# Kernel optimization log

Hardware: AMD Instinct MI355X
Metric: run time of the kernel (lower is better)

## Reference

```python
import jax, jax.numpy as jnp
import numpy as np
from jax import lax

K = 7            # cfg.network.PSROI_BINS == pool_size
FEAT_STRIDE = 16
LAMDA = 0.1
D_PER_BIN = 8    # feature channels per position-sensitive bin -> C = K*K*8 = 392


def _bilinear(feat, y, x, extra_idx):
    """Bilinearly sample feat[H,W,...] at float coords (y,x); extra_idx are
    integer index arrays (broadcast to y.shape) selecting trailing feat axes."""
    H, W = feat.shape[0], feat.shape[1]
    y0f = jnp.floor(y); x0f = jnp.floor(x)
    wy = (y - y0f)[..., None]
    wx = (x - x0f)[..., None]
    y0 = jnp.clip(y0f.astype(jnp.int32), 0, H - 1)
    y1 = jnp.clip(y0f.astype(jnp.int32) + 1, 0, H - 1)
    x0 = jnp.clip(x0f.astype(jnp.int32), 0, W - 1)
    x1 = jnp.clip(x0f.astype(jnp.int32) + 1, 0, W - 1)
    def g(yi, xi):
        return feat[(yi, xi) + extra_idx]
    return ((1 - wy) * (1 - wx) * g(y0, x0) + (1 - wy) * wx * g(y0, x1)
            + wy * (1 - wx) * g(y1, x0) + wy * wx * g(y1, x1))


def ps_roi(f, rois, k, feat_stride, offsets=None):
    """Position-sensitive RoI pooling. f: [H,W,C] with C = k*k*D (bin-major
    channel layout). rois: [N,5] (batch, x1, y1, x2, y2) in image coords.
    offsets (optional): [N, k*k, G, 2] per-bin, per-channel-group (x,y) shifts
    in image coords. Returns [N, D, k, k]."""
    H, W, C = f.shape
    N = rois.shape[0]
    kk = k * k
    D = C // kk
    x1 = rois[:, 1] / feat_stride
    y1 = rois[:, 2] / feat_stride
    x2 = (rois[:, 3] + 1.0) / feat_stride
    y2 = (rois[:, 4] + 1.0) / feat_stride
    bw = (x2 - x1) / k  # [N]
    bh = (y2 - y1) / k
    jj = jnp.tile(jnp.arange(k, dtype=f.dtype), k)     # bin = i*k + j
    ii = jnp.repeat(jnp.arange(k, dtype=f.dtype), k)
    cx = x1[:, None] + (jj + 0.5) * bw[:, None]        # [N, kk] bin centers
    cy = y1[:, None] + (ii + 0.5) * bh[:, None]
    bins = jnp.arange(kk, dtype=jnp.int32)
    if offsets is None:
        feat = f.reshape(H, W, kk, D)
        b = jnp.broadcast_to(bins, (N, kk))
        vals = _bilinear(feat, cy, cx, (b,))           # [N, kk, D]
    else:
        G = offsets.shape[2]
        cxg = cx[:, :, None] + offsets[..., 0] / feat_stride  # [N, kk, G]
        cyg = cy[:, :, None] + offsets[..., 1] / feat_stride
        feat = f.reshape(H, W, kk, G, D // G)
        b = jnp.broadcast_to(bins[None, :, None], (N, kk, G))
        g = jnp.broadcast_to(jnp.arange(G, dtype=jnp.int32)[None, None, :], (N, kk, G))
        vals = _bilinear(feat, cyg, cxg, (b, g))       # [N, kk, G, D//G]
        vals = vals.reshape(N, kk, D)
    return jnp.transpose(vals.reshape(N, k, k, D), (0, 3, 1, 2))  # [N, D, k, k]


def setup_inputs():
    key = jax.random.key(0)
    kf, kw, k1, k2 = jax.random.split(key, 4)
    H = W = 128
    C = K * K * D_PER_BIN
    N = 2048
    features = jax.random.normal(kf, (1, H, W, C), jnp.float32)
    conv_w = jax.random.normal(kw, (3, 3, C, 2 * 4 * K * K), jnp.float32) * 0.01
    img = float(H * FEAT_STRIDE)
    xy1 = jax.random.uniform(k1, (N, 2), minval=0.0, maxval=img * 0.6)
    wh = jax.random.uniform(k2, (N, 2), minval=32.0, maxval=img * 0.4)
    xy2 = jnp.minimum(xy1 + wh, img - 1.0)
    rois = jnp.concatenate([jnp.zeros((N, 1)), xy1[:, :1], xy1[:, 1:], xy2[:, :1], xy2[:, 1:]], axis=1).astype(jnp.float32)
    return {"features": features, "rois": rois, "conv_w": conv_w}


def reference(features, rois, conv_w):
    # offset branch: 3x3 conv (no bias) -> PS-RoI pool -> scale by lamda*roi size
    offset_map = lax.conv_general_dilated(features, conv_w, (1, 1), 'SAME',
                                          dimension_numbers=('NHWC', 'HWIO', 'NHWC'))
    off = ps_roi(offset_map[0], rois, K, FEAT_STRIDE)          # [N, 8, K, K]
    N = off.shape[0]
    off = off.reshape(N, -1, 2, K, K)                          # [N, 4, 2, K, K]
    off = jnp.transpose(off, (2, 3, 4, 1, 0))                  # [2, K, K, 4, N]
    roi_w = rois[:, 3] - rois[:, 1] + 1.0
    roi_h = rois[:, 4] - rois[:, 2] + 1.0
    off = jnp.stack((off[0] * roi_w * LAMDA, off[1] * roi_h * LAMDA), axis=0)
    off = jnp.transpose(off, (4, 1, 2, 3, 0))                  # [N, K, K, 4, 2]
    off = off.reshape(N, K * K, -1, 2)                         # [N, kk, 4, 2]
    # deformable PS-RoI pooling of the features with predicted offsets
    return ps_roi(features[0], rois, K, FEAT_STRIDE, offsets=off)  # [N, 8, K, K]
```

## Files before the change

kernel.cpp:

```cpp
#include <hip/hip_runtime.h>
#include <cstddef>
#include <cstdint>

#define HH    128
#define WW    128
#define CC    392
#define NPIX  (HH*WW)
#define NROI  2048
#define PSK   7
#define NBIN  49
#define LAMDA 0.1f

#define CPAD      448
#define HPAD      130
#define NPADCO    448
#define SEGSTRIDE (9*CPAD)
#define BKK       64

#define FBM 64
#define FBN 64
#define FBK 32

typedef _Float16 half8   __attribute__((ext_vector_type(8)));
typedef _Float16 half2v  __attribute__((ext_vector_type(2)));
typedef float    floatx4 __attribute__((ext_vector_type(4)));

__device__ __forceinline__ void async_ld16(const _Float16* g, _Float16* l) {
  __builtin_amdgcn_global_load_lds((const __attribute__((address_space(1))) void*)g,
                                   (__attribute__((address_space(3))) void*)l,
                                   16, 0, 0);
}

#define FPREP ((HPAD * HPAD * (CPAD / 8) + 255) / 256)
#define WPREP (9 * 14 * 14)

__global__ __launch_bounds__(256)
void prep_kernel(const float* __restrict__ F, const float* __restrict__ Wt,
                 _Float16* __restrict__ Fh, _Float16* __restrict__ Bth) {
  __shared__ float tile[32][33];
  const int t = threadIdx.x;
  if (blockIdx.x < FPREP) {
    const int idx = blockIdx.x * 256 + t;
    const int total = HPAD * HPAD * (CPAD / 8);
    if (idx >= total) return;
    const int p  = idx / (CPAD / 8);
    const int cg = idx - p * (CPAD / 8);
    const int c  = cg * 8;
    const int py = p / HPAD;
    const int px = p - py * HPAD;
    half8 h;
#pragma unroll
    for (int i = 0; i < 8; ++i) h[i] = (_Float16)0.f;
    if (py >= 1 && py <= HH && px >= 1 && px <= WW && c < CC) {
      const float* src = F + ((size_t)(py - 1) * WW + (px - 1)) * CC + c;
      const float4 v0 = *(const float4*)src;
      const float4 v1 = *(const float4*)(src + 4);
      h[0] = (_Float16)v0.x; h[1] = (_Float16)v0.y;
      h[2] = (_Float16)v0.z; h[3] = (_Float16)v0.w;
      h[4] = (_Float16)v1.x; h[5] = (_Float16)v1.y;
      h[6] = (_Float16)v1.z; h[7] = (_Float16)v1.w;
    }
    *(half8*)(Fh + (size_t)p * CPAD + c) = h;
  } else {
    const int bid = blockIdx.x - FPREP;
    const int seg = bid / (14 * 14);
    const int rem = bid - seg * (14 * 14);
    const int cit = rem / 14;
    const int cot = rem - cit * 14;
    const int ci0 = cit * 32, co0 = cot * 32;
#pragma unroll
    for (int i = 0; i < 4; ++i) {
      const int idx = t + i * 256;
      const int lr = idx >> 5;
      const int lc = idx & 31;
      const int ci = ci0 + lr, co = co0 + lc;
      float v = 0.f;
      if (ci < CC && co < CC) v = Wt[((size_t)seg * CC + ci) * CC + co];
      tile[lr][lc] = v;
    }
    __syncthreads();
#pragma unroll
    for (int i = 0; i < 4; ++i) {
      const int idx = t + i * 256;
      const int lr = idx >> 5;
      const int lc = idx & 31;
      Bth[(size_t)(co0 + lr) * SEGSTRIDE + seg * CPAD + ci0 + lc] = (_Float16)tile[lc][lr];
    }
  }
}

__global__ __launch_bounds__(256, 4)
void conv_mfma_kernel(const _Float16* __restrict__ Fh, const _Float16* __restrict__ Bth,
                      _Float16* __restrict__ OM) {
  __shared__ __align__(16) _Float16 As[128 * BKK];
  __shared__ __align__(16) _Float16 Bs[64 * BKK];

  const int t = threadIdx.x;
  const int L = t & 63;
  const int w = t >> 6;
  const int row0 = blockIdx.x * 128;
  const int col0 = blockIdx.y * 64;

  const int srow = L >> 3;
  const int kofs = ((L & 7) ^ srow) * 8;

  const int ya = row0 >> 7;
  const int nbase = col0 + w * 16 + srow;

  const int wm = (w >> 1) * 64;
  const int wn = (w & 1) * 32;
  const int fr = L & 15;
  const int quad = L >> 4;
  const int pg0 = (quad ^ (fr & 7)) * 8;
  const int pg1 = ((4 + quad) ^ (fr & 7)) * 8;

  floatx4 acc[4][2];
#pragma unroll
  for (int i = 0; i < 4; ++i)
#pragma unroll
    for (int j = 0; j < 2; ++j) {
      floatx4 z = {0.f, 0.f, 0.f, 0.f};
      acc[i][j] = z;
    }

  for (int q = 0; q < 63; ++q) {
    const int seg = q / 7;
    const int it  = q - seg * 7;
    const int dy = seg / 3 - 1;
    const int dx = seg - (seg / 3) * 3 - 1;
    const int fy = ya + 1 + dy;
    const int cb = it * BKK;
    const _Float16* gArow = Fh + ((size_t)fy * HPAD + (1 + dx)) * CPAD + kofs + cb;
    const _Float16* gB = Bth + (size_t)nbase * SEGSTRIDE + seg * CPAD + kofs + cb;

#pragma unroll
    for (int j = 0; j < 4; ++j) {
      const int xr = w * 32 + j * 8 + srow;
      async_ld16(gArow + (size_t)xr * CPAD, &As[(w * 32 + j * 8) * BKK]);
    }
#pragma unroll
    for (int j = 0; j < 2; ++j) {
      async_ld16(gB + (size_t)(j * 8) * SEGSTRIDE, &Bs[(w * 16 + j * 8) * BKK]);
    }
    __syncthreads();

    half8 a0[4], a1[4], b0[2], b1[2];
#pragma unroll
    for (int mt = 0; mt < 4; ++mt) {
      const int rb = (wm + mt * 16 + fr) * BKK;
      a0[mt] = *(const half8*)(&As[rb + pg0]);
      a1[mt] = *(const half8*)(&As[rb + pg1]);
    }
#pragma unroll
    for (int nt = 0; nt < 2; ++nt) {
      const int rb = (wn + nt * 16 + fr) * BKK;
      b0[nt] = *(const half8*)(&Bs[rb + pg0]);
      b1[nt] = *(const half8*)(&Bs[rb + pg1]);
    }
#pragma unroll
    for (int mt = 0; mt < 4; ++mt)
#pragma unroll
      for (int nt = 0; nt < 2; ++nt)
        acc[mt][nt] = __builtin_amdgcn_mfma_f32_16x16x32_f16(a0[mt], b0[nt], acc[mt][nt], 0, 0, 0);
#pragma unroll
    for (int mt = 0; mt < 4; ++mt)
#pragma unroll
      for (int nt = 0; nt < 2; ++nt)
        acc[mt][nt] = __builtin_amdgcn_mfma_f32_16x16x32_f16(a1[mt], b1[nt], acc[mt][nt], 0, 0, 0);
    __syncthreads();
  }

#pragma unroll
  for (int mt = 0; mt < 4; ++mt) {
    const int rbase = row0 + wm + mt * 16 + quad * 4;
#pragma unroll
    for (int nt = 0; nt < 2; ++nt) {
      const int col = col0 + wn + nt * 16 + fr;
      if (col < CC) {
#pragma unroll
        for (int r = 0; r < 4; ++r)
          OM[(size_t)(rbase + r) * CC + col] = (_Float16)acc[mt][nt][r];
      }
    }
  }
}

__global__ __launch_bounds__(256)
void conv3x3_kernel(const float* __restrict__ F, const float* __restrict__ Wt,
                    float* __restrict__ OM) {
  __shared__ float Asf[FBK][FBM + 4];
  __shared__ float Bsf[FBK][FBN + 4];

  const int t = threadIdx.x;
  const int ty = t >> 4;
  const int tx = t & 15;
  const int row0 = blockIdx.x * FBM;
  const int col0 = blockIdx.y * FBN;

  float acc[4][4];
#pragma unroll
  for (int i = 0; i < 4; ++i)
#pragma unroll
    for (int j = 0; j < 4; ++j) acc[i][j] = 0.f;

  for (int kc = 0; kc < 117; ++kc) {
    const int seg   = kc / 13;
    const int cbase = (kc - seg * 13) * FBK;
    const int dy    = seg / 3 - 1;
    const int dx    = seg - (seg / 3) * 3 - 1;

#pragma unroll
    for (int rep = 0; rep < (FBM * FBK) / 256; ++rep) {
      const int idx = t + rep * 256;
      const int r  = idx >> 5;
      const int lk = idx & 31;
      const int m  = row0 + r;
      const int y  = m >> 7, x = m & 127;
      const int yy = y + dy, xx = x + dx;
      const int ci = cbase + lk;
      float v = 0.f;
      if ((unsigned)yy < HH && (unsigned)xx < WW && ci < CC)
        v = F[((size_t)(yy * WW + xx)) * CC + ci];
      Asf[lk][r] = v;
    }
#pragma unroll
    for (int rep = 0; rep < (FBK * FBN) / 256; ++rep) {
      const int idx = t + rep * 256;
      const int lk  = idx >> 6;
      const int nn  = idx & 63;
      const int ci  = cbase + lk;
      const int col = col0 + nn;
      float v = 0.f;
      if (ci < CC && col < CC)
        v = Wt[((size_t)(seg * CC + ci)) * CC + col];
      Bsf[lk][nn] = v;
    }
    __syncthreads();

#pragma unroll
    for (int lk = 0; lk < FBK; ++lk) {
      const float4 a4 = *(const float4*)(&Asf[lk][ty * 4]);
      const float4 b4 = *(const float4*)(&Bsf[lk][tx * 4]);
      const float av[4] = {a4.x, a4.y, a4.z, a4.w};
      const float bv[4] = {b4.x, b4.y, b4.z, b4.w};
#pragma unroll
      for (int i = 0; i < 4; ++i)
#pragma unroll
        for (int j = 0; j < 4; ++j)
          acc[i][j] = fmaf(av[i], bv[j], acc[i][j]);
    }
    __syncthreads();
  }

  const int col = col0 + tx * 4;
  if (col < CC) {
#pragma unroll
    for (int i = 0; i < 4; ++i) {
      float4 v = make_float4(acc[i][0], acc[i][1], acc[i][2], acc[i][3]);
      *(float4*)(&OM[((size_t)(row0 + ty * 4 + i)) * CC + col]) = v;
    }
  }
}

__device__ __forceinline__ void bilin_setup(float y, float x,
                                            int& iy0, int& iy1, int& ix0, int& ix1,
                                            float& w00, float& w01, float& w10, float& w11) {
  const float y0f = floorf(y), x0f = floorf(x);
  const float wy = y - y0f, wx = x - x0f;
  const int a = (int)y0f, b = (int)x0f;
  iy0 = min(max(a, 0), HH - 1);
  iy1 = min(max(a + 1, 0), HH - 1);
  ix0 = min(max(b, 0), WW - 1);
  ix1 = min(max(b + 1, 0), WW - 1);
  w00 = (1.f - wy) * (1.f - wx);
  w01 = (1.f - wy) * wx;
  w10 = wy * (1.f - wx);
  w11 = wy * wx;
}

__device__ __forceinline__ void roi_geom(const float* R, int n, int bi, int bj,
                                         float& cx, float& cy, float& sxs, float& sys) {
  const float rx1 = R[n * 5 + 1], ry1 = R[n * 5 + 2];
  const float rx2 = R[n * 5 + 3], ry2 = R[n * 5 + 4];
  const float x1 = rx1 * (1.f / 16.f);
  const float y1 = ry1 * (1.f / 16.f);
  const float x2 = (rx2 + 1.f) * (1.f / 16.f);
  const float y2 = (ry2 + 1.f) * (1.f / 16.f);
  const float bw = (x2 - x1) * (1.f / 7.f);
  const float bh = (y2 - y1) * (1.f / 7.f);
  cx = x1 + ((float)bj + 0.5f) * bw;
  cy = y1 + ((float)bi + 0.5f) * bh;
  sxs = (rx2 - rx1 + 1.f) * (LAMDA / 16.f);
  sys = (ry2 - ry1 + 1.f) * (LAMDA / 16.f);
}

__global__ __launch_bounds__(256)
void psroi_pool_f16_kernel(const _Float16* __restrict__ Fh, const float* __restrict__ R,
                           const _Float16* __restrict__ OM, float* __restrict__ out) {
  const int tid = blockIdx.x * 256 + threadIdx.x;
  if (tid >= NROI * NBIN * 4) return;
  const int g  = tid & 3;
  const int nb = tid >> 2;
  const int n  = nb / NBIN;
  const int b  = nb - n * NBIN;
  const int bi = b / PSK;
  const int bj = b - bi * PSK;

  float cx, cy, sxs, sys;
  roi_geom(R, n, bi, bj, cx, cy, sxs, sys);

  int iy0, iy1, ix0, ix1;
  float w00, w01, w10, w11;
  bilin_setup(cy, cx, iy0, iy1, ix0, ix1, w00, w01, w10, w11);

  const size_t c0 = (size_t)b * 8 + 2 * g;
  const half2v m00 = *(const half2v*)(OM + (size_t)(iy0 * WW + ix0) * CC + c0);
  const half2v m01 = *(const half2v*)(OM + (size_t)(iy0 * WW + ix1) * CC + c0);
  const half2v m10 = *(const half2v*)(OM + (size_t)(iy1 * WW + ix0) * CC + c0);
  const half2v m11 = *(const half2v*)(OM + (size_t)(iy1 * WW + ix1) * CC + c0);

  const float ox = w00 * (float)m00[0] + w01 * (float)m01[0]
                 + w10 * (float)m10[0] + w11 * (float)m11[0];
  const float oy = w00 * (float)m00[1] + w01 * (float)m01[1]
                 + w10 * (float)m10[1] + w11 * (float)m11[1];

  const float sx = cx + ox * sxs;
  const float sy = cy + oy * sys;

  int jy0, jy1, jx0, jx1;
  float u00, u01, u10, u11;
  bilin_setup(sy, sx, jy0, jy1, jx0, jx1, u00, u01, u10, u11);

  const half2v q00 = *(const half2v*)(Fh + ((size_t)(jy0 + 1) * HPAD + (jx0 + 1)) * CPAD + c0);
  const half2v q01 = *(const half2v*)(Fh + ((size_t)(jy0 + 1) * HPAD + (jx1 + 1)) * CPAD + c0);
  const half2v q10 = *(const half2v*)(Fh + ((size_t)(jy1 + 1) * HPAD + (jx0 + 1)) * CPAD + c0);
  const half2v q11 = *(const half2v*)(Fh + ((size_t)(jy1 + 1) * HPAD + (jx1 + 1)) * CPAD + c0);

  const float v0 = u00 * (float)q00[0] + u01 * (float)q01[0]
                 + u10 * (float)q10[0] + u11 * (float)q11[0];
  const float v1 = u00 * (float)q00[1] + u01 * (float)q01[1]
                 + u10 * (float)q10[1] + u11 * (float)q11[1];

  out[((size_t)n * 8 + 2 * g + 0) * NBIN + b] = v0;
  out[((size_t)n * 8 + 2 * g + 1) * NBIN + b] = v1;
}

__global__ __launch_bounds__(256)
void psroi_pool_f32_kernel(const float* __restrict__ F, const float* __restrict__ R,
                           const float* __restrict__ OM, float* __restrict__ out) {
  const int tid = blockIdx.x * 256 + threadIdx.x;
  if (tid >= NROI * NBIN * 4) return;
  const int g  = tid & 3;
  const int nb = tid >> 2;
  const int n  = nb / NBIN;
  const int b  = nb - n * NBIN;
  const int bi = b / PSK;
  const int bj = b - bi * PSK;

  float cx, cy, sxs, sys;
  roi_geom(R, n, bi, bj, cx, cy, sxs, sys);

  int iy0, iy1, ix0, ix1;
  float w00, w01, w10, w11;
  bilin_setup(cy, cx, iy0, iy1, ix0, ix1, w00, w01, w10, w11);

  const size_t c0 = (size_t)b * 8 + 2 * g;
  const float2 m00 = *(const float2*)(OM + (size_t)(iy0 * WW + ix0) * CC + c0);
  const float2 m01 = *(const float2*)(OM + (size_t)(iy0 * WW + ix1) * CC + c0);
  const float2 m10 = *(const float2*)(OM + (size_t)(iy1 * WW + ix0) * CC + c0);
  const float2 m11 = *(const float2*)(OM + (size_t)(iy1 * WW + ix1) * CC + c0);

  const float ox = w00 * m00.x + w01 * m01.x + w10 * m10.x + w11 * m11.x;
  const float oy = w00 * m00.y + w01 * m01.y + w10 * m10.y + w11 * m11.y;

  const float sx = cx + ox * sxs;
  const float sy = cy + oy * sys;

  int jy0, jy1, jx0, jx1;
  float u00, u01, u10, u11;
  bilin_setup(sy, sx, jy0, jy1, jx0, jx1, u00, u01, u10, u11);

  const float2 q00 = *(const float2*)(F + (size_t)(jy0 * WW + jx0) * CC + c0);
  const float2 q01 = *(const float2*)(F + (size_t)(jy0 * WW + jx1) * CC + c0);
  const float2 q10 = *(const float2*)(F + (size_t)(jy1 * WW + jx0) * CC + c0);
  const float2 q11 = *(const float2*)(F + (size_t)(jy1 * WW + jx1) * CC + c0);

  const float v0 = u00 * q00.x + u01 * q01.x + u10 * q10.x + u11 * q11.x;
  const float v1 = u00 * q00.y + u01 * q01.y + u10 * q10.y + u11 * q11.y;

  out[((size_t)n * 8 + 2 * g + 0) * NBIN + b] = v0;
  out[((size_t)n * 8 + 2 * g + 1) * NBIN + b] = v1;
}

extern "C" void kernel_launch(void* const* d_in, const int* in_sizes, int n_in,
                              void* d_out, int out_size, void* d_ws, size_t ws_size,
                              hipStream_t stream) {
  const float* F  = (const float*)d_in[0];
  const float* R  = (const float*)d_in[1];
  const float* Wt = (const float*)d_in[2];
  float* out = (float*)d_out;

  const size_t omBytes  = (size_t)NPIX * CC * sizeof(_Float16);
  const size_t fhBytes  = (size_t)HPAD * HPAD * CPAD * sizeof(_Float16);
  const size_t bthBytes = (size_t)NPADCO * SEGSTRIDE * sizeof(_Float16);
  const size_t need = omBytes + fhBytes + bthBytes;

  const int totalPool = NROI * NBIN * 4;
  const int poolGrid = (totalPool + 255) / 256;

  if (ws_size >= need) {
    _Float16* OM  = (_Float16*)d_ws;
    _Float16* Fh  = (_Float16*)((char*)d_ws + omBytes);
    _Float16* Bth = Fh + (size_t)HPAD * HPAD * CPAD;

    prep_kernel<<<FPREP + WPREP, 256, 0, stream>>>(F, Wt, Fh, Bth);

    dim3 g(NPIX / 128, NPADCO / 64);
    conv_mfma_kernel<<<g, 256, 0, stream>>>(Fh, Bth, OM);

    psroi_pool_f16_kernel<<<poolGrid, 256, 0, stream>>>(Fh, R, OM, out);
  } else {
    float* OMf = (float*)d_ws;
    dim3 cgrid(NPIX / FBM, (CC + FBN - 1) / FBN);
    conv3x3_kernel<<<cgrid, 256, 0, stream>>>(F, Wt, OMf);
    psroi_pool_f32_kernel<<<poolGrid, 256, 0, stream>>>(F, R, OMf, out);
  }
}
```

Measured before the change: 164.6 us.

## Enlarge conv MFMA tile to 128x128 and split K across two partial outputs

The conv GEMM tile is widened to 128 output channels per block and the 63 K-iterations are split across a z-dimension of two, each writing a separate fp16 partial offset map. The pooling kernel reads both partial maps and sums them during the offset bilinear interpolation. This aims to improve operand reuse per block and raise parallelism per block's K length. In exchange, padding output channels to 512 wastes more MFMA work, the larger accumulator array raises register pressure, and a second offset map must be written.

After: 167.4 us. Within noise of the previous version (+1.7%).

```diff
diff --git a/kernel.cpp b/kernel.cpp
--- a/kernel.cpp
+++ b/kernel.cpp
@@ -13,9 +13,10 @@
 
 #define CPAD      448
 #define HPAD      130
-#define NPADCO    448
+#define NPADCO    512
 #define SEGSTRIDE (9*CPAD)
 #define BKK       64
+#define NQ        63
 
 #define FBM 64
 #define FBN 64
@@ -32,7 +33,7 @@
 }
 
 #define FPREP ((HPAD * HPAD * (CPAD / 8) + 255) / 256)
-#define WPREP (9 * 14 * 14)
+#define WPREP (9 * 14 * 16)
 
 __global__ __launch_bounds__(256)
 void prep_kernel(const float* __restrict__ F, const float* __restrict__ Wt,
@@ -63,10 +64,10 @@
     *(half8*)(Fh + (size_t)p * CPAD + c) = h;
   } else {
     const int bid = blockIdx.x - FPREP;
-    const int seg = bid / (14 * 14);
-    const int rem = bid - seg * (14 * 14);
-    const int cit = rem / 14;
-    const int cot = rem - cit * 14;
+    const int seg = bid / (14 * 16);
+    const int rem = bid - seg * (14 * 16);
+    const int cit = rem / 16;
+    const int cot = rem - cit * 16;
     const int ci0 = cit * 32, co0 = cot * 32;
 #pragma unroll
     for (int i = 0; i < 4; ++i) {
@@ -91,39 +92,43 @@
 
 __global__ __launch_bounds__(256, 4)
 void conv_mfma_kernel(const _Float16* __restrict__ Fh, const _Float16* __restrict__ Bth,
-                      _Float16* __restrict__ OM) {
+                      _Float16* __restrict__ OMbase, int span) {
   __shared__ __align__(16) _Float16 As[128 * BKK];
-  __shared__ __align__(16) _Float16 Bs[64 * BKK];
+  __shared__ __align__(16) _Float16 Bs[128 * BKK];
 
   const int t = threadIdx.x;
   const int L = t & 63;
   const int w = t >> 6;
   const int row0 = blockIdx.x * 128;
-  const int col0 = blockIdx.y * 64;
+  const int col0 = blockIdx.y * 128;
+  const int kz   = blockIdx.z;
+  const int q0 = kz * span;
+  const int q1 = min(NQ, q0 + span);
+  _Float16* __restrict__ OMp = OMbase + (size_t)kz * NPIX * CC;
 
   const int srow = L >> 3;
   const int kofs = ((L & 7) ^ srow) * 8;
 
   const int ya = row0 >> 7;
-  const int nbase = col0 + w * 16 + srow;
+  const int nbase = col0 + w * 32 + srow;
 
   const int wm = (w >> 1) * 64;
-  const int wn = (w & 1) * 32;
+  const int wn = (w & 1) * 64;
   const int fr = L & 15;
   const int quad = L >> 4;
   const int pg0 = (quad ^ (fr & 7)) * 8;
   const int pg1 = ((4 + quad) ^ (fr & 7)) * 8;
 
-  floatx4 acc[4][2];
+  floatx4 acc[4][4];
 #pragma unroll
   for (int i = 0; i < 4; ++i)
 #pragma unroll
-    for (int j = 0; j < 2; ++j) {
+    for (int j = 0; j < 4; ++j) {
       floatx4 z = {0.f, 0.f, 0.f, 0.f};
       acc[i][j] = z;
     }
 
-  for (int q = 0; q < 63; ++q) {
+  for (int q = q0; q < q1; ++q) {
     const int seg = q / 7;
     const int it  = q - seg * 7;
     const int dy = seg / 3 - 1;
@@ -139,12 +144,12 @@
       async_ld16(gArow + (size_t)xr * CPAD, &As[(w * 32 + j * 8) * BKK]);
     }
 #pragma unroll
-    for (int j = 0; j < 2; ++j) {
-      async_ld16(gB + (size_t)(j * 8) * SEGSTRIDE, &Bs[(w * 16 + j * 8) * BKK]);
+    for (int j = 0; j < 4; ++j) {
+      async_ld16(gB + (size_t)(j * 8) * SEGSTRIDE, &Bs[(w * 32 + j * 8) * BKK]);
     }
     __syncthreads();
 
-    half8 a0[4], a1[4], b0[2], b1[2];
+    half8 a0[4], a1[4], b0[4], b1[4];
 #pragma unroll
     for (int mt = 0; mt < 4; ++mt) {
       const int rb = (wm + mt * 16 + fr) * BKK;
@@ -152,7 +157,7 @@
       a1[mt] = *(const half8*)(&As[rb + pg1]);
     }
 #pragma unroll
-    for (int nt = 0; nt < 2; ++nt) {
+    for (int nt = 0; nt < 4; ++nt) {
       const int rb = (wn + nt * 16 + fr) * BKK;
       b0[nt] = *(const half8*)(&Bs[rb + pg0]);
       b1[nt] = *(const half8*)(&Bs[rb + pg1]);
@@ -160,12 +165,12 @@
 #pragma unroll
     for (int mt = 0; mt < 4; ++mt)
 #pragma unroll
-      for (int nt = 0; nt < 2; ++nt)
+      for (int nt = 0; nt < 4; ++nt)
         acc[mt][nt] = __builtin_amdgcn_mfma_f32_16x16x32_f16(a0[mt], b0[nt], acc[mt][nt], 0, 0, 0);
 #pragma unroll
     for (int mt = 0; mt < 4; ++mt)
 #pragma unroll
-      for (int nt = 0; nt < 2; ++nt)
+      for (int nt = 0; nt < 4; ++nt)
         acc[mt][nt] = __builtin_amdgcn_mfma_f32_16x16x32_f16(a1[mt], b1[nt], acc[mt][nt], 0, 0, 0);
     __syncthreads();
   }
@@ -174,12 +179,12 @@
   for (int mt = 0; mt < 4; ++mt) {
     const int rbase = row0 + wm + mt * 16 + quad * 4;
 #pragma unroll
-    for (int nt = 0; nt < 2; ++nt) {
+    for (int nt = 0; nt < 4; ++nt) {
       const int col = col0 + wn + nt * 16 + fr;
       if (col < CC) {
 #pragma unroll
         for (int r = 0; r < 4; ++r)
-          OM[(size_t)(rbase + r) * CC + col] = (_Float16)acc[mt][nt][r];
+          OMp[(size_t)(rbase + r) * CC + col] = (_Float16)acc[mt][nt][r];
       }
     }
   }
@@ -296,7 +301,8 @@
 
 __global__ __launch_bounds__(256)
 void psroi_pool_f16_kernel(const _Float16* __restrict__ Fh, const float* __restrict__ R,
-                           const _Float16* __restrict__ OM, float* __restrict__ out) {
+                           const _Float16* __restrict__ OMa, const _Float16* __restrict__ OMb,
+                           float* __restrict__ out) {
   const int tid = blockIdx.x * 256 + threadIdx.x;
   if (tid >= NROI * NBIN * 4) return;
   const int g  = tid & 3;
@@ -314,15 +320,28 @@
   bilin_setup(cy, cx, iy0, iy1, ix0, ix1, w00, w01, w10, w11);
 
   const size_t c0 = (size_t)b * 8 + 2 * g;
-  const half2v m00 = *(const half2v*)(OM + (size_t)(iy0 * WW + ix0) * CC + c0);
-  const half2v m01 = *(const half2v*)(OM + (size_t)(iy0 * WW + ix1) * CC + c0);
-  const half2v m10 = *(const half2v*)(OM + (size_t)(iy1 * WW + ix0) * CC + c0);
-  const half2v m11 = *(const half2v*)(OM + (size_t)(iy1 * WW + ix1) * CC + c0);
-
-  const float ox = w00 * (float)m00[0] + w01 * (float)m01[0]
-                 + w10 * (float)m10[0] + w11 * (float)m11[0];
-  const float oy = w00 * (float)m00[1] + w01 * (float)m01[1]
-                 + w10 * (float)m10[1] + w11 * (float)m11[1];
+  const size_t s00 = (size_t)(iy0 * WW + ix0) * CC + c0;
+  const size_t s01 = (size_t)(iy0 * WW + ix1) * CC + c0;
+  const size_t s10 = (size_t)(iy1 * WW + ix0) * CC + c0;
+  const size_t s11 = (size_t)(iy1 * WW + ix1) * CC + c0;
+
+  const half2v a00 = *(const half2v*)(OMa + s00);
+  const half2v a01 = *(const half2v*)(OMa + s01);
+  const half2v a10 = *(const half2v*)(OMa + s10);
+  const half2v a11 = *(const half2v*)(OMa + s11);
+  const half2v e00 = *(const half2v*)(OMb + s00);
+  const half2v e01 = *(const half2v*)(OMb + s01);
+  const half2v e10 = *(const half2v*)(OMb + s10);
+  const half2v e11 = *(const half2v*)(OMb + s11);
+
+  const float ox = w00 * ((float)a00[0] + (float)e00[0])
+                 + w01 * ((float)a01[0] + (float)e01[0])
+                 + w10 * ((float)a10[0] + (float)e10[0])
+                 + w11 * ((float)a11[0] + (float)e11[0]);
+  const float oy = w00 * ((float)a00[1] + (float)e00[1])
+                 + w01 * ((float)a01[1] + (float)e01[1])
+                 + w10 * ((float)a10[1] + (float)e10[1])
+                 + w11 * ((float)a11[1] + (float)e11[1]);
 
   const float sx = cx + ox * sxs;
   const float sy = cy + oy * sys;
@@ -403,22 +422,23 @@
   const size_t omBytes  = (size_t)NPIX * CC * sizeof(_Float16);
   const size_t fhBytes  = (size_t)HPAD * HPAD * CPAD * sizeof(_Float16);
   const size_t bthBytes = (size_t)NPADCO * SEGSTRIDE * sizeof(_Float16);
-  const size_t need = omBytes + fhBytes + bthBytes;
+  const size_t need = 2 * omBytes + fhBytes + bthBytes;
 
   const int totalPool = NROI * NBIN * 4;
   const int poolGrid = (totalPool + 255) / 256;
 
   if (ws_size >= need) {
-    _Float16* OM  = (_Float16*)d_ws;
-    _Float16* Fh  = (_Float16*)((char*)d_ws + omBytes);
+    _Float16* OMa = (_Float16*)d_ws;
+    _Float16* OMb = OMa + (size_t)NPIX * CC;
+    _Float16* Fh  = (_Float16*)((char*)d_ws + 2 * omBytes);
     _Float16* Bth = Fh + (size_t)HPAD * HPAD * CPAD;
 
     prep_kernel<<<FPREP + WPREP, 256, 0, stream>>>(F, Wt, Fh, Bth);
 
-    dim3 g(NPIX / 128, NPADCO / 64);
-    conv_mfma_kernel<<<g, 256, 0, stream>>>(Fh, Bth, OM);
-
-    psroi_pool_f16_kernel<<<poolGrid, 256, 0, stream>>>(Fh, R, OM, out);
+    dim3 g(NPIX / 128, NPADCO / 128, 2);
+    conv_mfma_kernel<<<g, 256, 0, stream>>>(Fh, Bth, OMa, 32);
+
+    psroi_pool_f16_kernel<<<poolGrid, 256, 0, stream>>>(Fh, R, OMa, OMb, out);
   } else {
     float* OMf = (float*)d_ws;
     dim3 cgrid(NPIX / FBM, (CC + FBN - 1) / FBN);
```
